# Optimization experiments

Measured on AMD Instinct MI355X. Metric: run time of the kernel, lower is better.

The kernel has to match this reference:

```python
import jax, jax.numpy as jnp
import numpy as np

DEPTH = 3


def _outer(a, b):
    # batched tensor product of flattened tensor-algebra levels: (B, m) x (B, n) -> (B, m*n)
    return (a[:, :, None] * b[:, None, :]).reshape(a.shape[0], -1)


def _signature(X, depth):
    """Truncated path signature via Chen's identity (matches signatory.signature,
    basepoint=False). X: (B, T, C) -> (B, sum_k C^k)."""
    B, T, C = X.shape
    dX = X[:, 1:, :] - X[:, :-1, :]  # (B, T-1, C) increments

    def exp_levels(dx):
        # exp(dx) in truncated tensor algebra: level k = dx^{\otimes k} / k!
        e = [dx]
        for k in range(2, depth + 1):
            e.append(_outer(e[-1], dx) / k)
        return e

    def step(S, dx):
        e = exp_levels(dx)
        new = []
        for k in range(1, depth + 1):
            t = S[k - 1] + e[k - 1]  # terms with S_0=1 or e_0=1
            for i in range(1, k):
                t = t + _outer(S[i - 1], e[k - i - 1])
            new.append(t)
        return tuple(new), None

    init = tuple(jnp.zeros((B, C ** k), X.dtype) for k in range(1, depth + 1))
    S, _ = jax.lax.scan(step, init, jnp.swapaxes(dX, 0, 1))  # scan over time
    return jnp.concatenate(S, axis=1)


def setup_inputs() -> dict:
    key = jax.random.key(0)
    kx, kw, kb = jax.random.split(key, 3)
    B, T, C, n_out = 2048, 128, 8, 10
    sig_dim = sum(C ** k for k in range(1, DEPTH + 1))  # 584
    X = jax.random.normal(kx, (B, T, C), dtype=jnp.float32)
    bound = 1.0 / np.sqrt(sig_dim)
    W = jax.random.uniform(kw, (n_out, sig_dim), jnp.float32, -bound, bound)
    b = jax.random.uniform(kb, (n_out,), jnp.float32, -bound, bound)
    return {"X": X, "W": W, "b": b}


def reference(X, W, b):
    sig = _signature(X, DEPTH)          # (B, sig_dim)
    out = sig @ W.T + b                  # (B, n_outputs)
    return out.reshape(-1, W.shape[0])
```

## Files before the change

kernel.cpp:

```cpp
#include <hip/hip_runtime.h>

#define NOUT 10
#define SIG_DIM 584
#define TPAD 132

typedef float float8v __attribute__((ext_vector_type(8)));

__device__ __forceinline__ float rdlane(float x, int lane) {
    return __int_as_float(__builtin_amdgcn_readlane(__float_as_int(x), lane));
}

__global__ __launch_bounds__(256) void dx_prepass(const float* __restrict__ X,
                                                  float* __restrict__ dX)
{
    const int t = blockIdx.x * 256 + threadIdx.x;
    const int r = (t >> 1) & 127;
    const float4* X4 = reinterpret_cast<const float4*>(X);
    const float4 a = X4[t];
    float4 d = make_float4(0.f, 0.f, 0.f, 0.f);
    if (r < 127) {
        const float4 c = X4[t + 2];
        d = make_float4(c.x - a.x, c.y - a.y, c.z - a.z, c.w - a.w);
    }
    reinterpret_cast<float4*>(dX)[t] = d;
}

__global__ __launch_bounds__(256) void sig_main(
    const float* __restrict__ X, const float* __restrict__ dX,
    const float* __restrict__ W, const float* __restrict__ bias,
    float* __restrict__ out)
{
    __shared__ float s_dxT[4][8 * TPAD];

    const int tid = threadIdx.x;
    const int w = tid >> 6;
    const int l = tid & 63;
    const int i = l >> 3;
    const int j = l & 7;
    const int b = blockIdx.x * 4 + w;
    const int bu = __builtin_amdgcn_readfirstlane(b);
    const float* dXb = dX + (size_t)bu * 1024;

    float* dxT = &s_dxT[w][0];
    const int cb = (l & 1) * 4;
    const int rl = l >> 1;
#pragma unroll
    for (int q = 0; q < 4; ++q) {
        const int r = q * 32 + rl;
        const float4 d = *reinterpret_cast<const float4*>(dXb + r * 8 + cb);
        dxT[(cb + 0) * TPAD + r] = d.x;
        dxT[(cb + 1) * TPAD + r] = d.y;
        dxT[(cb + 2) * TPAD + r] = d.z;
        dxT[(cb + 3) * TPAD + r] = d.w;
    }
    __syncthreads();

    float s3[8];
#pragma unroll
    for (int k = 0; k < 8; ++k) s3[k] = 0.f;
    float s2 = 0.f, s1i = 0.f;

    const float* icol = dxT + i * TPAD;
    const float* jcol = dxT + j * TPAD;
    const float8v* srow = reinterpret_cast<const float8v*>(dXb);

#define STEP(T, DXI, DXJ)                                                     \
    {                                                                         \
        const float8v rr = srow[(T)];              \
        const float cc = (DXI) * (DXJ);                                       \
        const float uu = s1i * (DXJ);                                         \
        const float f  = fmaf(0.5f, uu, fmaf(1.0f / 6.0f, cc, s2));           \
        s3[0] = fmaf(f, rr[0], s3[0]);                                        \
        s3[1] = fmaf(f, rr[1], s3[1]);                                        \
        s3[2] = fmaf(f, rr[2], s3[2]);                                        \
        s3[3] = fmaf(f, rr[3], s3[3]);                                        \
        s3[4] = fmaf(f, rr[4], s3[4]);                                        \
        s3[5] = fmaf(f, rr[5], s3[5]);                                        \
        s3[6] = fmaf(f, rr[6], s3[6]);                                        \
        s3[7] = fmaf(f, rr[7], s3[7]);                                        \
        s2 = fmaf(0.5f, cc, s2 + uu);                                         \
        s1i += (DXI);                                                         \
    }

#define GROUP(T0)                                                             \
    {                                                                         \
        const float4 ic = *reinterpret_cast<const float4*>(icol + (T0));      \
        const float4 jc = *reinterpret_cast<const float4*>(jcol + (T0));      \
        STEP((T0) + 0, ic.x, jc.x)                                            \
        STEP((T0) + 1, ic.y, jc.y)                                            \
        STEP((T0) + 2, ic.z, jc.z)                                            \
        STEP((T0) + 3, ic.w, jc.w)                                            \
    }
#define G16(A) GROUP(A) GROUP((A) + 4) GROUP((A) + 8) GROUP((A) + 12)
    G16(0) G16(16) G16(32) G16(48) G16(64) G16(80) G16(96) G16(112)
#undef G16
#undef GROUP
#undef STEP

    const float* Xb = X + (size_t)b * 1024;
    const float s1j = Xb[127 * 8 + j] - Xb[j];

#pragma unroll
    for (int o = 0; o < NOUT; ++o) {
        const float* wrow = W + o * SIG_DIM;
        float part = s2 * wrow[8 + l];
        const float4 w0 = *reinterpret_cast<const float4*>(wrow + 72 + l * 8);
        const float4 w1 = *reinterpret_cast<const float4*>(wrow + 72 + l * 8 + 4);
        part = fmaf(s3[0], w0.x, part); part = fmaf(s3[1], w0.y, part);
        part = fmaf(s3[2], w0.z, part); part = fmaf(s3[3], w0.w, part);
        part = fmaf(s3[4], w1.x, part); part = fmaf(s3[5], w1.y, part);
        part = fmaf(s3[6], w1.z, part); part = fmaf(s3[7], w1.w, part);
        if (i == 0) part = fmaf(s1j, wrow[j], part);
#pragma unroll
        for (int off = 32; off > 0; off >>= 1) part += __shfl_xor(part, off);
        if (l == 0) out[b * NOUT + o] = part + bias[o];
    }
}

__global__ __launch_bounds__(256) void sig_fallback(
    const float* __restrict__ X, const float* __restrict__ W,
    const float* __restrict__ bias, float* __restrict__ out)
{
    __shared__ float s_dxT[4][8 * TPAD];
    const int tid = threadIdx.x;
    const int w = tid >> 6;
    const int l = tid & 63;
    const int i = l >> 3;
    const int j = l & 7;
    const int b = blockIdx.x * 4 + w;
    const float* Xb = X + (size_t)b * 1024;
    float* dxT = &s_dxT[w][0];
    const int cb = (l & 1) * 4;
    const int rl = l >> 1;
    float4 dA, dB, dC, dD;
#define PREP(DQ, QQ)                                                          \
    {                                                                         \
        const int r = (QQ) * 32 + rl;                                         \
        const float* xr = Xb + r * 8 + cb;                                    \
        const float4 a  = *reinterpret_cast<const float4*>(xr);               \
        const float4 c4 = *reinterpret_cast<const float4*>(xr + (r < 127 ? 8 : 0)); \
        DQ.x = (r < 127) ? c4.x - a.x : 0.f;                                  \
        DQ.y = (r < 127) ? c4.y - a.y : 0.f;                                  \
        DQ.z = (r < 127) ? c4.z - a.z : 0.f;                                  \
        DQ.w = (r < 127) ? c4.w - a.w : 0.f;                                  \
        dxT[(cb + 0) * TPAD + r] = DQ.x;                                      \
        dxT[(cb + 1) * TPAD + r] = DQ.y;                                      \
        dxT[(cb + 2) * TPAD + r] = DQ.z;                                      \
        dxT[(cb + 3) * TPAD + r] = DQ.w;                                      \
    }
    PREP(dA, 0) PREP(dB, 1) PREP(dC, 2) PREP(dD, 3)
#undef PREP
    __syncthreads();
    float s3[8];
#pragma unroll
    for (int k = 0; k < 8; ++k) s3[k] = 0.f;
    float s2 = 0.f, s1i = 0.f, s1j = 0.f;
    const float* icol = dxT + i * TPAD;
    const float* jcol = dxT + j * TPAD;
#define STEP(DQ, LB, DXI, DXJ)                                                \
    {                                                                         \
        const float k0 = rdlane(DQ.x, (LB));                                  \
        const float k1 = rdlane(DQ.y, (LB));                                  \
        const float k2 = rdlane(DQ.z, (LB));                                  \
        const float k3 = rdlane(DQ.w, (LB));                                  \
        const float k4 = rdlane(DQ.x, (LB) + 1);                              \
        const float k5 = rdlane(DQ.y, (LB) + 1);                              \
        const float k6 = rdlane(DQ.z, (LB) + 1);                              \
        const float k7 = rdlane(DQ.w, (LB) + 1);                              \
        const float cc = (DXI) * (DXJ);                                       \
        const float uu = s1i * (DXJ);                                         \
        const float f  = fmaf(0.5f, uu, fmaf(1.0f / 6.0f, cc, s2));           \
        s3[0] = fmaf(f, k0, s3[0]);                                           \
        s3[1] = fmaf(f, k1, s3[1]);                                           \
        s3[2] = fmaf(f, k2, s3[2]);                                           \
        s3[3] = fmaf(f, k3, s3[3]);                                           \
        s3[4] = fmaf(f, k4, s3[4]);                                           \
        s3[5] = fmaf(f, k5, s3[5]);                                           \
        s3[6] = fmaf(f, k6, s3[6]);                                           \
        s3[7] = fmaf(f, k7, s3[7]);                                           \
        s2 = fmaf(0.5f, cc, s2 + uu);                                         \
        s1i += (DXI);                                                         \
        s1j += (DXJ);                                                         \
    }
#define SECTION(DQ, QQ)                                                       \
    for (int g = 0; g < 8; ++g) {                                             \
        const int t0 = (QQ) * 32 + g * 4;                                     \
        const float4 ic = *reinterpret_cast<const float4*>(icol + t0);        \
        const float4 jc = *reinterpret_cast<const float4*>(jcol + t0);        \
        const int lb = g * 8;                                                 \
        STEP(DQ, lb + 0, ic.x, jc.x)                                          \
        STEP(DQ, lb + 2, ic.y, jc.y)                                          \
        STEP(DQ, lb + 4, ic.z, jc.z)                                          \
        STEP(DQ, lb + 6, ic.w, jc.w)                                          \
    }
    SECTION(dA, 0) SECTION(dB, 1) SECTION(dC, 2) SECTION(dD, 3)
#undef SECTION
#undef STEP
#pragma unroll
    for (int o = 0; o < NOUT; ++o) {
        const float* wrow = W + o * SIG_DIM;
        float part = s2 * wrow[8 + l];
        const float4 w0 = *reinterpret_cast<const float4*>(wrow + 72 + l * 8);
        const float4 w1 = *reinterpret_cast<const float4*>(wrow + 72 + l * 8 + 4);
        part = fmaf(s3[0], w0.x, part); part = fmaf(s3[1], w0.y, part);
        part = fmaf(s3[2], w0.z, part); part = fmaf(s3[3], w0.w, part);
        part = fmaf(s3[4], w1.x, part); part = fmaf(s3[5], w1.y, part);
        part = fmaf(s3[6], w1.z, part); part = fmaf(s3[7], w1.w, part);
        if (i == 0) part = fmaf(s1j, wrow[j], part);
#pragma unroll
        for (int off = 32; off > 0; off >>= 1) part += __shfl_xor(part, off);
        if (l == 0) out[b * NOUT + o] = part + bias[o];
    }
}

extern "C" void kernel_launch(void* const* d_in, const int* in_sizes, int n_in,
                              void* d_out, int out_size, void* d_ws, size_t ws_size,
                              hipStream_t stream) {
    const float* X = (const float*)d_in[0];
    const float* W = (const float*)d_in[1];
    const float* bias = (const float*)d_in[2];
    float* out = (float*)d_out;
    const size_t need = 2048ull * 1024ull * sizeof(float);
    if (ws_size >= need) {
        float* dX = (float*)d_ws;
        dx_prepass<<<dim3(2048), dim3(256), 0, stream>>>(X, dX);
        sig_main<<<dim3(512), dim3(256), 0, stream>>>(X, dX, W, bias, out);
    } else {
        sig_fallback<<<dim3(512), dim3(256), 0, stream>>>(X, W, bias, out);
    }
}
```

Baseline: 25.17 us.

## Split each path's time scan across eight waves and merge with Chen's identity

Each batch element now gets its own 512-thread block. Each of its eight waves computes the signature of a 16-step time segment instead of one wave scanning all 128 steps serially. The partial signatures are published to LDS and combined in a three-level tree using Chen's identity. The final output dot products are spread across the waves. This trades a long serial dependency chain and low wave count for extra LDS traffic, block-wide barriers and merge arithmetic. It also uses float4 LDS reads at odd-stride (TPAD 17) offsets, which may be unaligned.

```diff
diff --git a/kernel.cpp b/kernel.cpp
--- a/kernel.cpp
+++ b/kernel.cpp
@@ -2,7 +2,8 @@
 
 #define NOUT 10
 #define SIG_DIM 584
-#define TPAD 132
+#define TPAD 17
+#define TPAD2 132
 
 typedef float float8v __attribute__((ext_vector_type(8)));
 
@@ -25,48 +26,48 @@
     reinterpret_cast<float4*>(dX)[t] = d;
 }
 
-__global__ __launch_bounds__(256) void sig_main(
-    const float* __restrict__ X, const float* __restrict__ dX,
-    const float* __restrict__ W, const float* __restrict__ bias,
-    float* __restrict__ out)
+__global__ __launch_bounds__(512) void sig_main(
+    const float* __restrict__ dX, const float* __restrict__ W,
+    const float* __restrict__ bias, float* __restrict__ out)
 {
-    __shared__ float s_dxT[4][8 * TPAD];
+    __shared__ float s_dxT[8][8 * TPAD];
+    __shared__ float s_sig[8][SIG_DIM];
+    __shared__ float s_sig2[4][SIG_DIM];
 
     const int tid = threadIdx.x;
     const int w = tid >> 6;
     const int l = tid & 63;
     const int i = l >> 3;
     const int j = l & 7;
-    const int b = blockIdx.x * 4 + w;
-    const int bu = __builtin_amdgcn_readfirstlane(b);
-    const float* dXb = dX + (size_t)bu * 1024;
-
-    float* dxT = &s_dxT[w][0];
-    const int cb = (l & 1) * 4;
-    const int rl = l >> 1;
-#pragma unroll
-    for (int q = 0; q < 4; ++q) {
-        const int r = q * 32 + rl;
-        const float4 d = *reinterpret_cast<const float4*>(dXb + r * 8 + cb);
-        dxT[(cb + 0) * TPAD + r] = d.x;
-        dxT[(cb + 1) * TPAD + r] = d.y;
-        dxT[(cb + 2) * TPAD + r] = d.z;
-        dxT[(cb + 3) * TPAD + r] = d.w;
-    }
+    const int b = blockIdx.x;
+    const int t0 = w * 16;
+
+    const float* dXb = dX + (size_t)b * 1024;
+
+    if (l < 32) {
+        const float4 d = *reinterpret_cast<const float4*>(dXb + t0 * 8 + l * 4);
+        float* dt = &s_dxT[w][0];
+        const int r = l >> 1, cb = (l & 1) * 4;
+        dt[(cb + 0) * TPAD + r] = d.x;
+        dt[(cb + 1) * TPAD + r] = d.y;
+        dt[(cb + 2) * TPAD + r] = d.z;
+        dt[(cb + 3) * TPAD + r] = d.w;
+    }
+    const float8v* srow = reinterpret_cast<const float8v*>(
+        dX + (size_t)__builtin_amdgcn_readfirstlane(b * 1024 + t0 * 8));
     __syncthreads();
 
     float s3[8];
 #pragma unroll
     for (int k = 0; k < 8; ++k) s3[k] = 0.f;
-    float s2 = 0.f, s1i = 0.f;
-
-    const float* icol = dxT + i * TPAD;
-    const float* jcol = dxT + j * TPAD;
-    const float8v* srow = reinterpret_cast<const float8v*>(dXb);
+    float s2 = 0.f, s1i = 0.f, s1j = 0.f;
+
+    const float* icol = &s_dxT[w][i * TPAD];
+    const float* jcol = &s_dxT[w][j * TPAD];
 
 #define STEP(T, DXI, DXJ)                                                     \
     {                                                                         \
-        const float8v rr = srow[(T)];              \
+        const float8v rr = srow[(T)];                                         \
         const float cc = (DXI) * (DXJ);                                       \
         const float uu = s1i * (DXJ);                                         \
         const float f  = fmaf(0.5f, uu, fmaf(1.0f / 6.0f, cc, s2));           \
@@ -80,28 +81,83 @@
         s3[7] = fmaf(f, rr[7], s3[7]);                                        \
         s2 = fmaf(0.5f, cc, s2 + uu);                                         \
         s1i += (DXI);                                                         \
-    }
-
-#define GROUP(T0)                                                             \
-    {                                                                         \
-        const float4 ic = *reinterpret_cast<const float4*>(icol + (T0));      \
-        const float4 jc = *reinterpret_cast<const float4*>(jcol + (T0));      \
-        STEP((T0) + 0, ic.x, jc.x)                                            \
-        STEP((T0) + 1, ic.y, jc.y)                                            \
-        STEP((T0) + 2, ic.z, jc.z)                                            \
-        STEP((T0) + 3, ic.w, jc.w)                                            \
-    }
-#define G16(A) GROUP(A) GROUP((A) + 4) GROUP((A) + 8) GROUP((A) + 12)
-    G16(0) G16(16) G16(32) G16(48) G16(64) G16(80) G16(96) G16(112)
-#undef G16
-#undef GROUP
+        s1j += (DXJ);                                                         \
+    }
+#pragma unroll
+    for (int g = 0; g < 4; ++g) {
+        const float4 ic = *reinterpret_cast<const float4*>(icol + g * 4);
+        const float4 jc = *reinterpret_cast<const float4*>(jcol + g * 4);
+        STEP(g * 4 + 0, ic.x, jc.x)
+        STEP(g * 4 + 1, ic.y, jc.y)
+        STEP(g * 4 + 2, ic.z, jc.z)
+        STEP(g * 4 + 3, ic.w, jc.w)
+    }
 #undef STEP
 
-    const float* Xb = X + (size_t)b * 1024;
-    const float s1j = Xb[127 * 8 + j] - Xb[j];
-
-#pragma unroll
-    for (int o = 0; o < NOUT; ++o) {
+#define PUBLISH(SG)                                                           \
+    {                                                                         \
+        float* sg_ = (SG);                                                    \
+        if (i == 0) sg_[j] = s1j;                                             \
+        sg_[8 + l] = s2;                                                      \
+        _Pragma("unroll")                                                     \
+        for (int k = 0; k < 8; ++k) sg_[72 + k * 64 + l] = s3[k];             \
+    }
+#define FOLDF(SG)                                                             \
+    {                                                                         \
+        const float* sg_ = (SG);                                              \
+        const float4 b0 = *reinterpret_cast<const float4*>(sg_);              \
+        const float4 b1 = *reinterpret_cast<const float4*>(sg_ + 4);          \
+        const float s1bi = sg_[i];                                            \
+        const float s1bj = sg_[j];                                            \
+        const float s2b = sg_[8 + l];                                         \
+        const float4 q0 = *reinterpret_cast<const float4*>(sg_ + 8 + j * 8);  \
+        const float4 q1 = *reinterpret_cast<const float4*>(sg_ + 8 + j * 8 + 4); \
+        float tb[8];                                                          \
+        _Pragma("unroll")                                                     \
+        for (int k = 0; k < 8; ++k) tb[k] = sg_[72 + k * 64 + l];             \
+        s3[0] = fmaf(s2, b0.x, fmaf(s1i, q0.x, s3[0] + tb[0]));               \
+        s3[1] = fmaf(s2, b0.y, fmaf(s1i, q0.y, s3[1] + tb[1]));               \
+        s3[2] = fmaf(s2, b0.z, fmaf(s1i, q0.z, s3[2] + tb[2]));               \
+        s3[3] = fmaf(s2, b0.w, fmaf(s1i, q0.w, s3[3] + tb[3]));               \
+        s3[4] = fmaf(s2, b1.x, fmaf(s1i, q1.x, s3[4] + tb[4]));               \
+        s3[5] = fmaf(s2, b1.y, fmaf(s1i, q1.y, s3[5] + tb[5]));               \
+        s3[6] = fmaf(s2, b1.z, fmaf(s1i, q1.z, s3[6] + tb[6]));               \
+        s3[7] = fmaf(s2, b1.w, fmaf(s1i, q1.w, s3[7] + tb[7]));               \
+        s2 = s2 + fmaf(s1i, s1bj, s2b);                                       \
+        s1i += s1bi;                                                          \
+        s1j += s1bj;                                                          \
+    }
+#define ZERO_STATE                                                            \
+    {                                                                         \
+        _Pragma("unroll")                                                     \
+        for (int k = 0; k < 8; ++k) s3[k] = 0.f;                              \
+        s2 = 0.f; s1i = 0.f; s1j = 0.f;                                       \
+    }
+
+    PUBLISH(&s_sig[w][0]);
+    __syncthreads();
+    if (w < 4) {
+        ZERO_STATE;
+        FOLDF(&s_sig[2 * w][0]);
+        FOLDF(&s_sig[2 * w + 1][0]);
+        PUBLISH(&s_sig2[w][0]);
+    }
+    __syncthreads();
+    if (w < 2) {
+        ZERO_STATE;
+        FOLDF(&s_sig2[2 * w][0]);
+        FOLDF(&s_sig2[2 * w + 1][0]);
+        PUBLISH(&s_sig[w][0]);
+    }
+    __syncthreads();
+    ZERO_STATE;
+    FOLDF(&s_sig[0][0]);
+    FOLDF(&s_sig[1][0]);
+#undef ZERO_STATE
+#undef FOLDF
+#undef PUBLISH
+
+    for (int o = w; o < NOUT; o += 8) {
         const float* wrow = W + o * SIG_DIM;
         float part = s2 * wrow[8 + l];
         const float4 w0 = *reinterpret_cast<const float4*>(wrow + 72 + l * 8);
@@ -121,7 +177,7 @@
     const float* __restrict__ X, const float* __restrict__ W,
     const float* __restrict__ bias, float* __restrict__ out)
 {
-    __shared__ float s_dxT[4][8 * TPAD];
+    __shared__ float s_dxT[4][8 * TPAD2];
     const int tid = threadIdx.x;
     const int w = tid >> 6;
     const int l = tid & 63;
@@ -143,10 +199,10 @@
         DQ.y = (r < 127) ? c4.y - a.y : 0.f;                                  \
         DQ.z = (r < 127) ? c4.z - a.z : 0.f;                                  \
         DQ.w = (r < 127) ? c4.w - a.w : 0.f;                                  \
-        dxT[(cb + 0) * TPAD + r] = DQ.x;                                      \
-        dxT[(cb + 1) * TPAD + r] = DQ.y;                                      \
-        dxT[(cb + 2) * TPAD + r] = DQ.z;                                      \
-        dxT[(cb + 3) * TPAD + r] = DQ.w;                                      \
+        dxT[(cb + 0) * TPAD2 + r] = DQ.x;                                     \
+        dxT[(cb + 1) * TPAD2 + r] = DQ.y;                                     \
+        dxT[(cb + 2) * TPAD2 + r] = DQ.z;                                     \
+        dxT[(cb + 3) * TPAD2 + r] = DQ.w;                                     \
     }
     PREP(dA, 0) PREP(dB, 1) PREP(dC, 2) PREP(dD, 3)
 #undef PREP
@@ -155,8 +211,8 @@
 #pragma unroll
     for (int k = 0; k < 8; ++k) s3[k] = 0.f;
     float s2 = 0.f, s1i = 0.f, s1j = 0.f;
-    const float* icol = dxT + i * TPAD;
-    const float* jcol = dxT + j * TPAD;
+    const float* icol = dxT + i * TPAD2;
+    const float* jcol = dxT + j * TPAD2;
 #define STEP(DQ, LB, DXI, DXJ)                                                \
     {                                                                         \
         const float k0 = rdlane(DQ.x, (LB));                                  \
@@ -224,7 +280,7 @@
     if (ws_size >= need) {
         float* dX = (float*)d_ws;
         dx_prepass<<<dim3(2048), dim3(256), 0, stream>>>(X, dX);
-        sig_main<<<dim3(512), dim3(256), 0, stream>>>(X, dX, W, bias, out);
+        sig_main<<<dim3(2048), dim3(512), 0, stream>>>(dX, W, bias, out);
     } else {
         sig_fallback<<<dim3(512), dim3(256), 0, stream>>>(X, W, bias, out);
     }
```

Measured after the change: 37.87 us. 50.4% more time.
